# Optimization experiments

Hardware: AMD Instinct MI355X
Metric: run time of the kernel (lower is better)

## Reference

```python
import jax, jax.numpy as jnp
import numpy as np

B, S, D, H, DFF = 2, 2048, 768, 12, 3072
DK = D // H
EPS = 1e-6


def setup_inputs() -> dict:
    key = jax.random.key(0)
    ks = jax.random.split(key, 12)
    n = lambda k, shp: jax.random.normal(k, shp, jnp.float32) * 0.02
    return {
        "x": jax.random.normal(ks[0], (B, S, D), jnp.float32),
        "mask": jax.random.randint(ks[1], (1, 1, S, S), 0, 2).astype(jnp.int32),
        "wq": n(ks[2], (D, D)), "bq": jnp.zeros((D,), jnp.float32),
        "wk": n(ks[3], (D, D)), "bk": jnp.zeros((D,), jnp.float32),
        "wv": n(ks[4], (D, D)), "bv": jnp.zeros((D,), jnp.float32),
        "wo": n(ks[5], (D, D)), "bo": jnp.zeros((D,), jnp.float32),
        "w1": n(ks[6], (D, DFF)), "b1": jnp.zeros((DFF,), jnp.float32),
        "w2": n(ks[7], (DFF, D)), "b2": jnp.zeros((D,), jnp.float32),
        "alpha1": jnp.ones((D,), jnp.float32), "beta1": jnp.zeros((D,), jnp.float32),
        "alpha2": jnp.ones((D,), jnp.float32), "beta2": jnp.zeros((D,), jnp.float32),
    }


def _layernorm(x, alpha, bias):
    # Faithful to source: unbiased std (ddof=1) and eps added to std, not var.
    mean = x.mean(axis=-1, keepdims=True)
    var = jnp.sum((x - mean) ** 2, axis=-1, keepdims=True) / (x.shape[-1] - 1)
    return alpha * (x - mean) / (jnp.sqrt(var) + EPS) + bias


def reference(x, mask, wq, bq, wk, bk, wv, bv, wo, bo, w1, b1, w2, b2,
              alpha1, beta1, alpha2, beta2):
    # --- residual 1: pre-norm self-attention ---
    h = _layernorm(x, alpha1, beta1)
    q = (h @ wq + bq).reshape(B, S, H, DK).transpose(0, 2, 1, 3)  # [B,H,S,DK]
    k = (h @ wk + bk).reshape(B, S, H, DK).transpose(0, 2, 1, 3)
    v = (h @ wv + bv).reshape(B, S, H, DK).transpose(0, 2, 1, 3)
    scores = jnp.einsum('bhsd,bhtd->bhst', q, k) / jnp.sqrt(jnp.float32(DK))
    scores = jnp.where(mask == 0, jnp.float32(-1e9), scores)
    attn = jax.nn.softmax(scores, axis=-1)
    o = jnp.einsum('bhst,bhtd->bhsd', attn, v)
    o = o.transpose(0, 2, 1, 3).reshape(B, S, D)
    x = x + (o @ wo + bo)
    # --- residual 2: pre-norm FFN ---
    h2 = _layernorm(x, alpha2, beta2)
    ff = jnp.maximum(h2 @ w1 + b1, 0.0) @ w2 + b2
    return x + ff
```

## Files before the change

### kernel.cpp

```cpp
#include <hip/hip_runtime.h>

typedef unsigned short u16;
typedef unsigned int u32;
typedef unsigned long long u64;
typedef __attribute__((ext_vector_type(8))) short bf16x8;
typedef __attribute__((ext_vector_type(4))) float f32x4;
typedef __attribute__((ext_vector_type(2))) unsigned int u32x2;

#define SEQ 2048
#define DM  768
#define NH  12
#define NB  2
#define LDQ (3 * DM)

#define SCALE_Q 0.180336879f
#define NEGB   -1.44269504e9f

__device__ __forceinline__ float bf2f(u16 u) {
  union { u32 i; float f; } v; v.i = ((u32)u) << 16; return v.f;
}
__device__ __forceinline__ u16 f2bf(float f) {
  union { float f; u32 i; } v; v.f = f;
  u32 r = v.i + 0x7FFFu + ((v.i >> 16) & 1u);
  return (u16)(r >> 16);
}
__device__ __forceinline__ float hw_exp2(float x) {
  float r;
  asm("v_exp_f32 %0, %1" : "=v"(r) : "v"(x));
  return r;
}
__device__ __forceinline__ void gl_lds16(const u16* g, u16* l) {
  __builtin_amdgcn_global_load_lds(
      (const __attribute__((address_space(1))) unsigned int*)g,
      (__attribute__((address_space(3))) unsigned int*)l, 16, 0, 0);
}
template<int N> __device__ __forceinline__ void wait_vmcnt() {
  if constexpr (N == 0) asm volatile("s_waitcnt vmcnt(0)" ::: "memory");
  else if constexpr (N == 3) asm volatile("s_waitcnt vmcnt(3)" ::: "memory");
  else if constexpr (N == 4) asm volatile("s_waitcnt vmcnt(4)" ::: "memory");
  else if constexpr (N == 5) asm volatile("s_waitcnt vmcnt(5)" ::: "memory");
}

__global__ __launch_bounds__(256) void prep_kernel(
    const float* __restrict__ wq, const float* __restrict__ wk,
    const float* __restrict__ wv, const float* __restrict__ wo,
    const float* __restrict__ w1, const float* __restrict__ w2,
    const float* __restrict__ bq, const float* __restrict__ bk,
    const float* __restrict__ bv, const int* __restrict__ mask,
    u16* __restrict__ wqkvt, u16* __restrict__ wot,
    u16* __restrict__ w1t, u16* __restrict__ w2t,
    float* __restrict__ bqkv, u64* __restrict__ mbitsT) {
  __shared__ float t[32][33];
  const int j = blockIdx.x, tid = threadIdx.x;
  const float* in = nullptr; u16* out = nullptr;
  int R = 0, C = 0, bx = 0, by = 0; float sc = 1.0f;
  if (j < 2304) {
    int which = j / 576, local = j % 576;
    in = which == 0 ? wq : which == 1 ? wk : which == 2 ? wv : wo;
    out = which == 3 ? wot : wqkvt + (size_t)which * DM * DM;
    sc = (which == 0) ? SCALE_Q : 1.0f;
    R = DM; C = DM; bx = local % 24; by = local / 24;
  } else if (j < 4608) {
    int local = j - 2304;
    in = w1; out = w1t; R = DM; C = 3072; bx = local % 96; by = local / 96;
  } else if (j < 6912) {
    int local = j - 4608;
    in = w2; out = w2t; R = 3072; C = DM; bx = local % 24; by = local / 24;
  } else if (j < 6921) {
    int i = (j - 6912) * 256 + tid;
    float v = (i < DM) ? bq[i] * SCALE_Q : (i < 2 * DM ? bk[i - DM] : bv[i - 2 * DM]);
    bqkv[i] = v;
    return;
  } else {
    int wid = (j - 6921) * 4 + (tid >> 6);
    int lane = tid & 63;
    int row = wid >> 5, word = wid & 31;
    int m = mask[(long)row * SEQ + word * 64 + lane];
    u64 bb = __ballot(m != 0);
    if (lane == 0) mbitsT[(long)word * SEQ + row] = bb;
    return;
  }
  long r0 = (long)by * 32, c0 = (long)bx * 32;
  int lc = tid & 31, wr = tid >> 5;
#pragma unroll
  for (int i = 0; i < 4; i++) {
    int row = wr + i * 8;
    t[row][lc] = in[(r0 + row) * C + c0 + lc];
  }
  __syncthreads();
#pragma unroll
  for (int i = 0; i < 4; i++) {
    int row = wr + i * 8;
    out[(c0 + row) * R + r0 + lc] = f2bf(t[lc][row] * sc);
  }
}

__global__ __launch_bounds__(256) void transpose_kernel(
    const u16* __restrict__ in, u16* __restrict__ out, int ldin, int R, int C) {
  __shared__ u16 t[32][33];
  long r0 = (long)blockIdx.y * 32, c0 = (long)blockIdx.x * 32;
  int lc = threadIdx.x & 31, wr = threadIdx.x >> 5;
#pragma unroll
  for (int i = 0; i < 4; i++) {
    int row = wr + i * 8;
    t[row][lc] = in[(r0 + row) * (long)ldin + c0 + lc];
  }
  __syncthreads();
#pragma unroll
  for (int i = 0; i < 4; i++) {
    int row = wr + i * 8;
    out[(c0 + row) * R + r0 + lc] = t[lc][row];
  }
}

__global__ __launch_bounds__(256) void ln_kernel(
    const float* __restrict__ x, const float* __restrict__ alpha,
    const float* __restrict__ beta, u16* __restrict__ out) {
  long row = blockIdx.x;
  const float* xr = x + row * DM;
  int tid = threadIdx.x;
  float v[3];
  float s = 0.f, sq = 0.f;
#pragma unroll
  for (int i = 0; i < 3; i++) {
    v[i] = xr[tid + i * 256];
    s += v[i]; sq += v[i] * v[i];
  }
#pragma unroll
  for (int off = 32; off >= 1; off >>= 1) {
    s += __shfl_down(s, off, 64);
    sq += __shfl_down(sq, off, 64);
  }
  __shared__ float ss[4], ssq[4];
  int wave = tid >> 6;
  if ((tid & 63) == 0) { ss[wave] = s; ssq[wave] = sq; }
  __syncthreads();
  float ts = ss[0] + ss[1] + ss[2] + ss[3];
  float tsq = ssq[0] + ssq[1] + ssq[2] + ssq[3];
  float mean = ts * (1.0f / (float)DM);
  float var = fmaxf((tsq - ts * mean) * (1.0f / (float)(DM - 1)), 0.0f);
  float inv = 1.0f / (sqrtf(var) + 1e-6f);
#pragma unroll
  for (int i = 0; i < 3; i++) {
    int c = tid + i * 256;
    out[row * DM + c] = f2bf(alpha[c] * (v[i] - mean) * inv + beta[c]);
  }
}

template<int BN>
__global__ __launch_bounds__(256, 2) void gemm_bt_kernel(
    const u16* __restrict__ A, const u16* __restrict__ Bt,
    const float* __restrict__ bias, const float* res,
    u16* Cb, float* Cf, int M, int N, int K, int Kld,
    int relu, int nx, int wgPerChunk) {
  constexpr int NJ = BN / 32;
  constexpr int L = (BN == 128) ? 4 : 3;
  __shared__ __align__(16) u16 As[3][128][32];
  __shared__ __align__(16) u16 Bs[3][BN][32];
  const int tid = threadIdx.x;
  const int lane = tid & 63, wave = tid >> 6;
  const int g = lane >> 4, lr = lane & 15;
  const int wm = (wave >> 1) * 64, wn = (wave & 1) * (BN / 2);
  const int o = blockIdx.x;
  int wg = (o & 7) * ((int)gridDim.x >> 3) + (o >> 3);
  int chunk = 0;
  if (wgPerChunk) { chunk = wg / wgPerChunk; wg -= chunk * wgPerChunk; }
  const int bx = wg % nx, by = wg / nx;
  const long m0 = (long)by * 128;
  const long n0 = (long)bx * BN;
  const int srow = tid >> 2;
  const int scol = (tid & 3) * 8;
  const long koff = (long)chunk * K;

  const u16* aSrc = A + (m0 + srow) * Kld + koff + scol;
  const u16* bSrc = Bt + (n0 + srow) * Kld + koff + scol;

  auto STAGE = [&](int buf, int t) {
    const int k0 = t * 32;
    gl_lds16(aSrc + k0, &As[buf][srow][scol]);
    gl_lds16(aSrc + (long)64 * Kld + k0, &As[buf][srow + 64][scol]);
    gl_lds16(bSrc + k0, &Bs[buf][srow][scol]);
    if (BN == 128) gl_lds16(bSrc + (long)64 * Kld + k0, &Bs[buf][srow + 64][scol]);
  };

  f32x4 acc[4][NJ];
#pragma unroll
  for (int i = 0; i < 4; i++)
#pragma unroll
    for (int j = 0; j < NJ; j++) acc[i][j] = (f32x4)0.0f;

  const int nk = K / 32;
  STAGE(0, 0);
  STAGE(1, 1);
  for (int t = 0; t < nk; t++) {
    const int cur = t % 3;
    if (t + 1 < nk) wait_vmcnt<L>(); else wait_vmcnt<0>();
    __builtin_amdgcn_sched_barrier(0);
    __builtin_amdgcn_s_barrier();
    bf16x8 af[4], bfr[NJ];
#pragma unroll
    for (int i = 0; i < 4; i++) af[i] = *(const bf16x8*)&As[cur][wm + i * 16 + lr][g * 8];
#pragma unroll
    for (int j = 0; j < NJ; j++) bfr[j] = *(const bf16x8*)&Bs[cur][wn + j * 16 + lr][g * 8];
#pragma unroll
    for (int i = 0; i < 4; i++)
#pragma unroll
      for (int j = 0; j < NJ; j++)
        acc[i][j] = __builtin_amdgcn_mfma_f32_16x16x32_bf16(af[i], bfr[j], acc[i][j], 0, 0, 0);
    if (t + 2 < nk) STAGE((t + 2) % 3, t + 2);
  }
#pragma unroll
  for (int j = 0; j < NJ; j++) {
    long col = n0 + wn + j * 16 + lr;
    float bv = (bias && chunk == 0) ? bias[col] : 0.0f;
#pragma unroll
    for (int i = 0; i < 4; i++) {
#pragma unroll
      for (int r = 0; r < 4; r++) {
        long row = m0 + wm + i * 16 + g * 4 + r;
        float v = acc[i][j][r] + bv;
        if (res) v += res[row * N + col];
        if (relu) v = fmaxf(v, 0.0f);
        if (wgPerChunk) atomicAdd(&Cf[row * N + col], v);
        else if (Cb)    Cb[row * N + col] = f2bf(v);
        else            Cf[row * N + col] = v;
      }
    }
  }
}

__global__ __launch_bounds__(256, 3) void attn_kernel(
    const u16* __restrict__ qkv, const u16* __restrict__ vt,
    const u64* __restrict__ mbitsT, u16* __restrict__ o_) {
  __shared__ __align__(16) u16 Ks[2][64][64];
  __shared__ __align__(16) u16 Vs[2][64][64];
  __shared__ __align__(16) u32 Ps32[4][16][36];
  const int o = blockIdx.x;
  const int wg = (o & 7) * 96 + (o >> 3);
  const int qt = wg & 31, h = (wg >> 5) % NH, b = wg / (32 * NH);
  const int tid = threadIdx.x;
  const int lane = tid & 63, wave = tid >> 6;
  const int g = lane >> 4, lr = lane & 15;
  const int qr0 = qt * 64 + wave * 16;
  const int NT = SEQ / 64;

  const u16* q = qkv;
  const u16* k = qkv + DM;

  const long qbase = ((long)(b * SEQ + qr0 + lr)) * LDQ + h * 64;
  bf16x8 qf0 = *(const bf16x8*)(q + qbase + g * 8);
  bf16x8 qf1 = *(const bf16x8*)(q + qbase + 32 + g * 8);

  bf16x8 onesf;
#pragma unroll
  for (int j = 0; j < 8; j++) onesf[j] = (short)0x3F80;

  f32x4 lsum = (f32x4)0.0f;
  f32x4 oacc[4];
#pragma unroll
  for (int d = 0; d < 4; d++) oacc[d] = (f32x4)0.0f;

  const int strow = tid >> 3;
  const int stcolb = (tid & 7) * 16;
  const int swzb = stcolb ^ ((strow & 7) << 4);
  const u16* ksrc = k + (long)b * SEQ * LDQ + h * 64 + (swzb >> 1);
  const u16* vsrc = vt + ((long)(h * 64 + strow)) * (NB * SEQ) + (long)b * SEQ + (swzb >> 1);
  const int sc16 = stcolb >> 1;

  auto STAGE = [&](int buf, int kt) {
    const u16* kr = ksrc + (long)(kt * 64 + strow) * LDQ;
    gl_lds16(kr, &Ks[buf][strow][sc16]);
    gl_lds16(kr + (long)32 * LDQ, &Ks[buf][strow + 32][sc16]);
    const u16* vr = vsrc + kt * 64;
    gl_lds16(vr, &Vs[buf][strow][sc16]);
    gl_lds16(vr + 32 * (NB * SEQ), &Vs[buf][strow + 32][sc16]);
  };

  const int rs = (lr & 7) << 3;
  const int c0 = (g * 8) ^ rs;
  const int c1 = (32 + g * 8) ^ rs;

  const u64* mrow = mbitsT + (qr0 + lr);

  u64 mb_cur = mrow[0];
  STAGE(0, 0);
  for (int kt = 0; kt < NT; kt++) {
    const int cur = kt & 1;
    u64 mb_new = 0;
    if (kt + 1 < NT) {
      mb_new = mrow[(long)(kt + 1) * SEQ];
      STAGE(cur ^ 1, kt + 1);
      wait_vmcnt<5>();
    } else {
      wait_vmcnt<0>();
    }
    __builtin_amdgcn_sched_barrier(0);
    __builtin_amdgcn_s_barrier();

    f32x4 sf[4];
    __builtin_amdgcn_s_setprio(1);
#pragma unroll
    for (int n = 0; n < 4; n++) {
      bf16x8 kb0 = *(const bf16x8*)&Ks[cur][n * 16 + lr][c0];
      bf16x8 kb1 = *(const bf16x8*)&Ks[cur][n * 16 + lr][c1];
      sf[n] = __builtin_amdgcn_mfma_f32_16x16x32_bf16(kb0, qf0, (f32x4)0.0f, 0, 0, 0);
      sf[n] = __builtin_amdgcn_mfma_f32_16x16x32_bf16(kb1, qf1, sf[n], 0, 0, 0);
    }
    __builtin_amdgcn_s_setprio(0);
    u64 tsh = mb_cur >> (4 * g);
    u32 mlo = (u32)tsh, mhi = (u32)(tsh >> 32);
#pragma unroll
    for (int n = 0; n < 4; n++) {
      u32 w = (n < 2) ? mlo : mhi;
#pragma unroll
      for (int r = 0; r < 4; r++) {
        u32 bit = 1u << (16 * (n & 1) + r);
        sf[n][r] = (w & bit) ? sf[n][r] : NEGB;
      }
    }
#pragma unroll
    for (int n = 0; n < 4; n++) {
      union { float f; u32 i; } p0, p1, p2, p3;
      p0.f = hw_exp2(sf[n][0]); p1.f = hw_exp2(sf[n][1]);
      p2.f = hw_exp2(sf[n][2]); p3.f = hw_exp2(sf[n][3]);
      u32 w0 = __builtin_amdgcn_perm(p1.i, p0.i, 0x07060302u);
      u32 w1 = __builtin_amdgcn_perm(p3.i, p2.i, 0x07060302u);
      *(u32x2*)&Ps32[wave][lr][8 * n + 2 * g] = (u32x2){w0, w1};
    }
    asm volatile("" ::: "memory");
    bf16x8 pf0 = *(const bf16x8*)&Ps32[wave][lr][4 * g];
    bf16x8 pf1 = *(const bf16x8*)&Ps32[wave][lr][16 + 4 * g];
    __builtin_amdgcn_s_setprio(1);
    lsum = __builtin_amdgcn_mfma_f32_16x16x32_bf16(onesf, pf0, lsum, 0, 0, 0);
    lsum = __builtin_amdgcn_mfma_f32_16x16x32_bf16(onesf, pf1, lsum, 0, 0, 0);
#pragma unroll
    for (int db = 0; db < 4; db++) {
      bf16x8 v0 = *(const bf16x8*)&Vs[cur][db * 16 + lr][c0];
      bf16x8 v1 = *(const bf16x8*)&Vs[cur][db * 16 + lr][c1];
      oacc[db] = __builtin_amdgcn_mfma_f32_16x16x32_bf16(v0, pf0, oacc[db], 0, 0, 0);
      oacc[db] = __builtin_amdgcn_mfma_f32_16x16x32_bf16(v1, pf1, oacc[db], 0, 0, 0);
    }
    __builtin_amdgcn_s_setprio(0);
    __builtin_amdgcn_sched_barrier(0);
    __builtin_amdgcn_s_barrier();
    mb_cur = mb_new;
  }
  float inv = 1.0f / lsum[0];
  long row = (long)b * SEQ + qr0 + lr;
#pragma unroll
  for (int db = 0; db < 4; db++) {
    u32 lo = ((u32)f2bf(oacc[db][1] * inv) << 16) | f2bf(oacc[db][0] * inv);
    u32 hi = ((u32)f2bf(oacc[db][3] * inv) << 16) | f2bf(oacc[db][2] * inv);
    *(u32x2*)(o_ + row * DM + h * 64 + db * 16 + g * 4) = (u32x2){lo, hi};
  }
}

extern "C" void kernel_launch(void* const* d_in, const int* in_sizes, int n_in,
                              void* d_out, int out_size, void* d_ws, size_t ws_size,
                              hipStream_t stream) {
  const float* x      = (const float*)d_in[0];
  const int*   mask   = (const int*)d_in[1];
  const float* wq     = (const float*)d_in[2];
  const float* bq     = (const float*)d_in[3];
  const float* wk     = (const float*)d_in[4];
  const float* bk     = (const float*)d_in[5];
  const float* wv     = (const float*)d_in[6];
  const float* bv     = (const float*)d_in[7];
  const float* wo     = (const float*)d_in[8];
  const float* bo     = (const float*)d_in[9];
  const float* w1     = (const float*)d_in[10];
  const float* b1     = (const float*)d_in[11];
  const float* w2     = (const float*)d_in[12];
  const float* b2     = (const float*)d_in[13];
  const float* alpha1 = (const float*)d_in[14];
  const float* beta1  = (const float*)d_in[15];
  const float* alpha2 = (const float*)d_in[16];
  const float* beta2  = (const float*)d_in[17];
  float* outf = (float*)d_out;

  char* ws = (char*)d_ws;
  size_t off = 0;
  auto alloc = [&](size_t bytes) {
    void* p = ws + off;
    off += (bytes + 255) & ~(size_t)255;
    return p;
  };
  const size_t DD = (size_t)DM * DM * 2;
  const size_t DF = (size_t)DM * 3072 * 2;
  const size_t ROWS = (size_t)NB * SEQ;
  const size_t ACT = ROWS * DM * 2;

  u16* wqkvt = (u16*)alloc(3 * DD);
  u16* wot   = (u16*)alloc(DD);
  u16* w1t   = (u16*)alloc(DF);
  u16* w2t   = (u16*)alloc(DF);
  float* bqkv = (float*)alloc(3 * DM * 4);
  u64* mbitsT = (u64*)alloc((size_t)(SEQ / 64) * SEQ * 8);
  u16* h     = (u16*)alloc(ACT);
  u16* qkv   = (u16*)alloc(ROWS * 3 * DM * 2);
  u16* vtb   = (u16*)alloc(ACT);
  u16* ob    = (u16*)alloc(ACT);
  u16* fb = qkv;
  u16* h2 = h;
  float* x1 = outf;

  dim3 blk(256);
  prep_kernel<<<dim3(23305), blk, 0, stream>>>(wq, wk, wv, wo, w1, w2, bq, bk, bv,
                                               mask, wqkvt, wot, w1t, w2t, bqkv, mbitsT);

  ln_kernel<<<ROWS, blk, 0, stream>>>(x, alpha1, beta1, h);
  gemm_bt_kernel<128><<<dim3(576), blk, 0, stream>>>(
      h, wqkvt, bqkv, nullptr, qkv, nullptr, 4096, 3 * DM, 768, 768, 0, 18, 0);
  transpose_kernel<<<dim3(24, 128), blk, 0, stream>>>(qkv + 2 * DM, vtb, LDQ, 4096, 768);
  attn_kernel<<<dim3(32 * NH * NB), blk, 0, stream>>>(qkv, vtb, mbitsT, ob);
  gemm_bt_kernel<64><<<dim3(384), blk, 0, stream>>>(
      ob, wot, bo, x, nullptr, x1, 4096, 768, 768, 768, 0, 12, 0);
  ln_kernel<<<ROWS, blk, 0, stream>>>(x1, alpha2, beta2, h2);
  gemm_bt_kernel<128><<<dim3(768), blk, 0, stream>>>(
      h2, w1t, b1, nullptr, fb, nullptr, 4096, 3072, 768, 768, 1, 24, 0);
  gemm_bt_kernel<64><<<dim3(768), blk, 0, stream>>>(
      fb, w2t, b2, nullptr, nullptr, outf, 4096, 768, 1536, 3072, 0, 12, 384);
}
```

Measured before the change: 208.0 us.

## Fuse V transpose into QKV GEMM epilogue and restructure attention barriers

```diff
diff --git a/kernel.cpp b/kernel.cpp
--- a/kernel.cpp
+++ b/kernel.cpp
@@ -95,24 +95,6 @@
   }
 }
 
-__global__ __launch_bounds__(256) void transpose_kernel(
-    const u16* __restrict__ in, u16* __restrict__ out, int ldin, int R, int C) {
-  __shared__ u16 t[32][33];
-  long r0 = (long)blockIdx.y * 32, c0 = (long)blockIdx.x * 32;
-  int lc = threadIdx.x & 31, wr = threadIdx.x >> 5;
-#pragma unroll
-  for (int i = 0; i < 4; i++) {
-    int row = wr + i * 8;
-    t[row][lc] = in[(r0 + row) * (long)ldin + c0 + lc];
-  }
-  __syncthreads();
-#pragma unroll
-  for (int i = 0; i < 4; i++) {
-    int row = wr + i * 8;
-    out[(c0 + row) * R + r0 + lc] = t[lc][row];
-  }
-}
-
 __global__ __launch_bounds__(256) void ln_kernel(
     const float* __restrict__ x, const float* __restrict__ alpha,
     const float* __restrict__ beta, u16* __restrict__ out) {
@@ -151,7 +133,7 @@
 __global__ __launch_bounds__(256, 2) void gemm_bt_kernel(
     const u16* __restrict__ A, const u16* __restrict__ Bt,
     const float* __restrict__ bias, const float* res,
-    u16* Cb, float* Cf, int M, int N, int K, int Kld,
+    u16* Cb, float* Cf, u16* Vt, int vcol0, int M, int N, int K, int Kld,
     int relu, int nx, int wgPerChunk) {
   constexpr int NJ = BN / 32;
   constexpr int L = (BN == 128) ? 4 : 3;
@@ -209,21 +191,32 @@
         acc[i][j] = __builtin_amdgcn_mfma_f32_16x16x32_bf16(af[i], bfr[j], acc[i][j], 0, 0, 0);
     if (t + 2 < nk) STAGE((t + 2) % 3, t + 2);
   }
+  const bool isV = (Vt != nullptr) && (n0 >= vcol0);
 #pragma unroll
   for (int j = 0; j < NJ; j++) {
     long col = n0 + wn + j * 16 + lr;
     float bv = (bias && chunk == 0) ? bias[col] : 0.0f;
 #pragma unroll
     for (int i = 0; i < 4; i++) {
+      float vals[4];
 #pragma unroll
       for (int r = 0; r < 4; r++) {
         long row = m0 + wm + i * 16 + g * 4 + r;
         float v = acc[i][j][r] + bv;
         if (res) v += res[row * N + col];
         if (relu) v = fmaxf(v, 0.0f);
-        if (wgPerChunk) atomicAdd(&Cf[row * N + col], v);
-        else if (Cb)    Cb[row * N + col] = f2bf(v);
-        else            Cf[row * N + col] = v;
+        vals[r] = v;
+        if (!isV) {
+          if (wgPerChunk)  atomicAdd(&Cf[row * N + col], v);
+          else if (Cb)     Cb[row * N + col] = f2bf(v);
+          else             Cf[row * N + col] = v;
+        }
+      }
+      if (isV) {
+        long row0 = m0 + wm + i * 16 + g * 4;
+        u32 lo = ((u32)f2bf(vals[1]) << 16) | f2bf(vals[0]);
+        u32 hi = ((u32)f2bf(vals[3]) << 16) | f2bf(vals[2]);
+        *(u32x2*)(Vt + (col - vcol0) * (long)(NB * SEQ) + row0) = (u32x2){lo, hi};
       }
     }
   }
@@ -286,16 +279,14 @@
   STAGE(0, 0);
   for (int kt = 0; kt < NT; kt++) {
     const int cur = kt & 1;
+    wait_vmcnt<0>();
+    __builtin_amdgcn_sched_barrier(0);
+    __builtin_amdgcn_s_barrier();
     u64 mb_new = 0;
     if (kt + 1 < NT) {
       mb_new = mrow[(long)(kt + 1) * SEQ];
       STAGE(cur ^ 1, kt + 1);
-      wait_vmcnt<5>();
-    } else {
-      wait_vmcnt<0>();
-    }
-    __builtin_amdgcn_sched_barrier(0);
-    __builtin_amdgcn_s_barrier();
+    }
 
     f32x4 sf[4];
     __builtin_amdgcn_s_setprio(1);
@@ -341,8 +332,6 @@
       oacc[db] = __builtin_amdgcn_mfma_f32_16x16x32_bf16(v1, pf1, oacc[db], 0, 0, 0);
     }
     __builtin_amdgcn_s_setprio(0);
-    __builtin_amdgcn_sched_barrier(0);
-    __builtin_amdgcn_s_barrier();
     mb_cur = mb_new;
   }
   float inv = 1.0f / lsum[0];
@@ -410,14 +399,13 @@
 
   ln_kernel<<<ROWS, blk, 0, stream>>>(x, alpha1, beta1, h);
   gemm_bt_kernel<128><<<dim3(576), blk, 0, stream>>>(
-      h, wqkvt, bqkv, nullptr, qkv, nullptr, 4096, 3 * DM, 768, 768, 0, 18, 0);
-  transpose_kernel<<<dim3(24, 128), blk, 0, stream>>>(qkv + 2 * DM, vtb, LDQ, 4096, 768);
+      h, wqkvt, bqkv, nullptr, qkv, nullptr, vtb, 2 * DM, 4096, 3 * DM, 768, 768, 0, 18, 0);
   attn_kernel<<<dim3(32 * NH * NB), blk, 0, stream>>>(qkv, vtb, mbitsT, ob);
   gemm_bt_kernel<64><<<dim3(384), blk, 0, stream>>>(
-      ob, wot, bo, x, nullptr, x1, 4096, 768, 768, 768, 0, 12, 0);
+      ob, wot, bo, x, nullptr, x1, nullptr, 0, 4096, 768, 768, 768, 0, 12, 0);
   ln_kernel<<<ROWS, blk, 0, stream>>>(x1, alpha2, beta2, h2);
   gemm_bt_kernel<128><<<dim3(768), blk, 0, stream>>>(
-      h2, w1t, b1, nullptr, fb, nullptr, 4096, 3072, 768, 768, 1, 24, 0);
+      h2, w1t, b1, nullptr, fb, nullptr, nullptr, 0, 4096, 3072, 768, 768, 1, 24, 0);
   gemm_bt_kernel<64><<<dim3(768), blk, 0, stream>>>(
-      fb, w2t, b2, nullptr, nullptr, outf, 4096, 768, 1536, 3072, 0, 12, 384);
-}
+      fb, w2t, b2, nullptr, nullptr, outf, nullptr, 0, 4096, 768, 1536, 3072, 0, 12, 384);
+}
```

Measured after the change: 204.2 us (median of 2 runs). No clear change (-1.8%).
